# Performance work log

Measured on AMD Instinct MI355X. Metric: run time of the kernel, lower is better.

Reference implementation:

```python
import jax, jax.numpy as jnp
import numpy as np

N = 65536
NUM_STATE = 128
NUM_HIDDEN = 256
NUM_EMBED = 128


def setup_inputs() -> dict:
    key = jax.random.key(0)
    ks = jax.random.split(key, 8)
    s1 = jax.random.normal(ks[0], (N, NUM_STATE), dtype=jnp.float32)
    s2 = jax.random.normal(ks[1], (N, NUM_STATE), dtype=jnp.float32)
    # kaiming_normal_(fan_in, linear): std = 1/sqrt(fan_in)
    W1 = jax.random.normal(ks[2], (NUM_HIDDEN, NUM_STATE), dtype=jnp.float32) / np.sqrt(NUM_STATE)
    b1 = jnp.zeros((NUM_HIDDEN,), dtype=jnp.float32)
    W2 = jax.random.normal(ks[3], (NUM_HIDDEN, NUM_HIDDEN), dtype=jnp.float32) / np.sqrt(NUM_HIDDEN)
    b2 = jnp.zeros((NUM_HIDDEN,), dtype=jnp.float32)
    W3 = jax.random.normal(ks[4], (NUM_EMBED, NUM_HIDDEN), dtype=jnp.float32) / np.sqrt(NUM_HIDDEN)
    b3 = jnp.zeros((NUM_EMBED,), dtype=jnp.float32)
    return {"s1": s1, "s2": s2, "W1": W1, "b1": b1, "W2": W2, "b2": b2, "W3": W3, "b3": b3}


def _embed(x, W1, b1, W2, b2, W3, b3):
    h = jax.nn.selu(x @ W1.T + b1)
    h = jax.nn.selu(h @ W2.T + b2)
    return h @ W3.T + b3  # [N, num_embedding]


def reference(s1, s2, W1, b1, W2, b2, W3, b3):
    e1 = _embed(s1, W1, b1, W2, b2, W3, b3)
    e2 = _embed(s2, W1, b1, W2, b2, W3, b3)
    # diag(e1 @ e2.T) == per-row dot product (same math, O(N*d) not O(N^2*d))
    dots = jnp.einsum('nd,nd->n', e1, e2)
    out = dots / (jnp.linalg.norm(e1, axis=1) * jnp.linalg.norm(e2, axis=1))
    out = (out + 1.0) / 2.0
    return jax.nn.sigmoid(out)
```

## Files before the change

kernel.cpp:

```cpp
#include <hip/hip_runtime.h>


typedef __bf16 bf16x8 __attribute__((ext_vector_type(8)));
typedef __bf16 bf16x4 __attribute__((ext_vector_type(4)));
typedef float  f32x4  __attribute__((ext_vector_type(4)));

constexpr int WS_W1 = 0;
constexpr int WS_W2 = 32768;
constexpr int WS_W3 = 98304;

__device__ __forceinline__ float selu_f(float x) {
    const float scale = 1.0507009873554805f;
    const float sa    = 1.7580993408473766f;
    float xp = fmaxf(x, 0.f);
    float xn = fminf(x, 0.f);
    return fmaf(scale, xp, sa * (__expf(xn) - 1.f));
}

template<int COLS>
__device__ __forceinline__ bf16x8 read_act(const __bf16* lds, int row, int kcol) {
    unsigned byte = (unsigned)((row * COLS + kcol) * 2) ^ ((unsigned)(row & 7) << 4);
    return *(const bf16x8*)((const char*)lds + byte);
}

template<bool SELU, int COLS>
__device__ __forceinline__ void store_act(__bf16* lds, int row, int col0, f32x4 a) {
    float v0 = a[0], v1 = a[1], v2 = a[2], v3 = a[3];
    if (SELU) { v0 = selu_f(v0); v1 = selu_f(v1); v2 = selu_f(v2); v3 = selu_f(v3); }
    bf16x4 u;
    u[0] = (__bf16)v0; u[1] = (__bf16)v1; u[2] = (__bf16)v2; u[3] = (__bf16)v3;
    unsigned byte = (unsigned)((row * COLS + col0) * 2) ^ ((unsigned)(row & 7) << 4);
    *(bf16x4*)((char*)lds + byte) = u;
}

__global__ void pack_weights_kernel(const float* __restrict__ W1,
                                    const float* __restrict__ W2,
                                    const float* __restrict__ W3,
                                    __bf16* __restrict__ ws) {
    int t = blockIdx.x * blockDim.x + threadIdx.x;
    const float* W; int K, KS, f, base;
    if (t < 4096)       { W = W1; K = 128; KS = 4; f = t;         base = WS_W1; }
    else if (t < 12288) { W = W2; K = 256; KS = 8; f = t - 4096;  base = WS_W2; }
    else                { W = W3; K = 256; KS = 8; f = t - 12288; base = WS_W3; }
    int lane = f & 63;
    int ks   = (f >> 6) % KS;
    int ct   = f / (64 * KS);
    int row  = ct * 16 + (lane & 15);
    int k0   = ks * 32 + (lane >> 4) * 8;
    const float* src = W + (size_t)row * K + k0;
    __bf16* dst = ws + base + (size_t)f * 8;
#pragma unroll
    for (int j = 0; j < 8; ++j) dst[j] = (__bf16)src[j];
}

__global__ __launch_bounds__(256, 3)
void embed_sim_kernel(const float* __restrict__ s1, const float* __restrict__ s2,
                      const float* __restrict__ b1, const float* __restrict__ b2,
                      const float* __restrict__ b3,
                      const __bf16* __restrict__ wf, float* __restrict__ out) {
    __shared__ __align__(16) __bf16 Xs[64 * 128];
    __shared__ __align__(16) __bf16 hA[64 * 256];

    const int tid  = threadIdx.x;
    const int wave = tid >> 6;
    const int lane = tid & 63;
    const int lr   = lane & 15;
    const int kg   = lane >> 4;
    const int p0   = blockIdx.x * 32;

    __bf16* h2hi = hA;
    __bf16* Es   = hA + 64 * 128;

#pragma unroll
    for (int it = 0; it < 4; ++it) {
        int idx = tid + it * 256;
        int row = idx >> 4;
        int k0  = (idx & 15) << 3;
        const float* src = (row < 32) ? (s1 + (size_t)(p0 + row) * 128 + k0)
                                      : (s2 + (size_t)(p0 + row - 32) * 128 + k0);
        float4 v0 = *(const float4*)(src);
        float4 v1 = *(const float4*)(src + 4);
        bf16x8 w;
        w[0] = (__bf16)v0.x; w[1] = (__bf16)v0.y; w[2] = (__bf16)v0.z; w[3] = (__bf16)v0.w;
        w[4] = (__bf16)v1.x; w[5] = (__bf16)v1.y; w[6] = (__bf16)v1.z; w[7] = (__bf16)v1.w;
        unsigned byte = (unsigned)((row * 128 + k0) * 2) ^ ((unsigned)(row & 7) << 4);
        *(bf16x8*)((char*)Xs + byte) = w;
    }
    __syncthreads();

    {
        bf16x8 wfr[4][4]; f32x4 bv[4];
#pragma unroll
        for (int ti = 0; ti < 4; ++ti) {
            int t = wave * 4 + ti;
#pragma unroll
            for (int ks = 0; ks < 4; ++ks)
                wfr[ti][ks] = *(const bf16x8*)(wf + WS_W1 + (size_t)((t * 4 + ks) * 64 + lane) * 8);
            bv[ti] = *(const f32x4*)(b1 + t * 16 + kg * 4);
        }
#pragma unroll
        for (int s = 0; s < 4; ++s) {
            const int row = s * 16 + lr;
            bf16x8 xfr[4];
#pragma unroll
            for (int ks = 0; ks < 4; ++ks) xfr[ks] = read_act<128>(Xs, row, ks * 32 + kg * 8);
#pragma unroll
            for (int ti = 0; ti < 4; ++ti) {
                f32x4 acc = bv[ti];
#pragma unroll
                for (int ks = 0; ks < 4; ++ks)
                    acc = __builtin_amdgcn_mfma_f32_16x16x32_bf16(wfr[ti][ks], xfr[ks], acc, 0, 0, 0);
                store_act<true, 256>(hA, row, (wave * 4 + ti) * 16 + kg * 4, acc);
            }
        }
    }
    __syncthreads();

    {
        f32x4 acc[4][4];
#pragma unroll
        for (int ti = 0; ti < 4; ++ti) {
            f32x4 b = *(const f32x4*)(b2 + (wave * 4 + ti) * 16 + kg * 4);
#pragma unroll
            for (int s = 0; s < 4; ++s) acc[ti][s] = b;
        }
#pragma unroll
        for (int kh = 0; kh < 2; ++kh) {
            bf16x8 wfr[4][4];
#pragma unroll
            for (int ti = 0; ti < 4; ++ti) {
                int t = wave * 4 + ti;
#pragma unroll
                for (int ks = 0; ks < 4; ++ks)
                    wfr[ti][ks] = *(const bf16x8*)(wf + WS_W2 + (size_t)((t * 8 + kh * 4 + ks) * 64 + lane) * 8);
            }
#pragma unroll
            for (int s = 0; s < 4; ++s) {
                const int row = s * 16 + lr;
                bf16x8 hfr[4];
#pragma unroll
                for (int ks = 0; ks < 4; ++ks)
                    hfr[ks] = read_act<256>(hA, row, kh * 128 + ks * 32 + kg * 8);
#pragma unroll
                for (int ti = 0; ti < 4; ++ti)
#pragma unroll
                    for (int ks = 0; ks < 4; ++ks)
                        acc[ti][s] = __builtin_amdgcn_mfma_f32_16x16x32_bf16(
                            wfr[ti][ks], hfr[ks], acc[ti][s], 0, 0, 0);
            }
        }
        if (wave < 2) {
#pragma unroll
            for (int ti = 0; ti < 4; ++ti)
#pragma unroll
                for (int s = 0; s < 4; ++s)
                    store_act<true, 128>(Xs, s * 16 + lr, (wave * 4 + ti) * 16 + kg * 4, acc[ti][s]);
        }
        __syncthreads();
        if (wave >= 2) {
#pragma unroll
            for (int ti = 0; ti < 4; ++ti)
#pragma unroll
                for (int s = 0; s < 4; ++s)
                    store_act<true, 128>(h2hi, s * 16 + lr, ((wave - 2) * 4 + ti) * 16 + kg * 4, acc[ti][s]);
        }
    }
    __syncthreads();

    {
        f32x4 acc[2][4];
#pragma unroll
        for (int ti = 0; ti < 2; ++ti) {
            f32x4 b = *(const f32x4*)(b3 + (wave * 2 + ti) * 16 + kg * 4);
#pragma unroll
            for (int s = 0; s < 4; ++s) acc[ti][s] = b;
        }
#pragma unroll
        for (int kh = 0; kh < 2; ++kh) {
            const __bf16* src = (kh == 0) ? Xs : h2hi;
            bf16x8 wfr[2][4];
#pragma unroll
            for (int ti = 0; ti < 2; ++ti) {
                int t = wave * 2 + ti;
#pragma unroll
                for (int ks = 0; ks < 4; ++ks)
                    wfr[ti][ks] = *(const bf16x8*)(wf + WS_W3 + (size_t)((t * 8 + kh * 4 + ks) * 64 + lane) * 8);
            }
#pragma unroll
            for (int s = 0; s < 4; ++s) {
                const int row = s * 16 + lr;
                bf16x8 hfr[4];
#pragma unroll
                for (int ks = 0; ks < 4; ++ks)
                    hfr[ks] = read_act<128>(src, row, ks * 32 + kg * 8);
#pragma unroll
                for (int ti = 0; ti < 2; ++ti)
#pragma unroll
                    for (int ks = 0; ks < 4; ++ks)
                        acc[ti][s] = __builtin_amdgcn_mfma_f32_16x16x32_bf16(
                            wfr[ti][ks], hfr[ks], acc[ti][s], 0, 0, 0);
            }
        }
#pragma unroll
        for (int ti = 0; ti < 2; ++ti)
#pragma unroll
            for (int s = 0; s < 4; ++s)
                store_act<false, 128>(Es, s * 16 + lr, (wave * 2 + ti) * 16 + kg * 4, acc[ti][s]);
    }
    __syncthreads();

    const int p  = tid >> 3;
    const int dg = tid & 7;
    float dot = 0.f, n1 = 0.f, n2 = 0.f;
#pragma unroll
    for (int half = 0; half < 2; ++half) {
        int d0 = dg * 16 + half * 8;
        unsigned by1 = (unsigned)((p * 128 + d0) * 2) ^ ((unsigned)(p & 7) << 4);
        unsigned by2 = (unsigned)(((p + 32) * 128 + d0) * 2) ^ ((unsigned)((p + 32) & 7) << 4);
        bf16x8 e1 = *(const bf16x8*)((const char*)Es + by1);
        bf16x8 e2 = *(const bf16x8*)((const char*)Es + by2);
#pragma unroll
        for (int j = 0; j < 8; ++j) {
            float a = (float)e1[j], b = (float)e2[j];
            dot = fmaf(a, b, dot);
            n1  = fmaf(a, a, n1);
            n2  = fmaf(b, b, n2);
        }
    }
#pragma unroll
    for (int off = 1; off < 8; off <<= 1) {
        dot += __shfl_xor(dot, off);
        n1  += __shfl_xor(n1,  off);
        n2  += __shfl_xor(n2,  off);
    }
    if (dg == 0) {
        float r = dot * rsqrtf(n1 * n2);
        float x = (r + 1.f) * 0.5f;
        out[p0 + p] = 1.f / (1.f + __expf(-x));
    }
}

extern "C" void kernel_launch(void* const* d_in, const int* in_sizes, int n_in,
                              void* d_out, int out_size, void* d_ws, size_t ws_size,
                              hipStream_t stream) {
    const float* s1 = (const float*)d_in[0];
    const float* s2 = (const float*)d_in[1];
    const float* W1 = (const float*)d_in[2];
    const float* b1 = (const float*)d_in[3];
    const float* W2 = (const float*)d_in[4];
    const float* b2 = (const float*)d_in[5];
    const float* W3 = (const float*)d_in[6];
    const float* b3 = (const float*)d_in[7];
    __bf16* wf = (__bf16*)d_ws;
    float*  outp = (float*)d_out;

    pack_weights_kernel<<<64, 256, 0, stream>>>(W1, W2, W3, wf);

    const int npairs = in_sizes[0] / 128;
    embed_sim_kernel<<<npairs / 32, 256, 0, stream>>>(s1, s2, b1, b2, b3, wf, outp);
}
```

Measured before the change: 58.22 us.

## Compute cosine similarity from MFMA accumulators and add setprio around MFMA blocks

The final embedding is no longer written to LDS as bf16 and re-read for the per-row dot and norms. Partial dot and norm sums are taken straight from the layer-3 accumulators, reduced across lanes with shuffles, then summed over the four waves through a small fp32 LDS buffer. MFMA sections are wrapped in s_setprio to favour matrix issue, and SELU is rewritten with exp2f and an fma. The cosine is now computed in fp32 rather than on bf16-rounded embeddings, at the cost of an extra cross-wave reduction step.

```diff
diff --git a/kernel.cpp b/kernel.cpp
--- a/kernel.cpp
+++ b/kernel.cpp
@@ -12,9 +12,9 @@
 __device__ __forceinline__ float selu_f(float x) {
     const float scale = 1.0507009873554805f;
     const float sa    = 1.7580993408473766f;
-    float xp = fmaxf(x, 0.f);
-    float xn = fminf(x, 0.f);
-    return fmaf(scale, xp, sa * (__expf(xn) - 1.f));
+    const float l2e   = 1.4426950408889634f;
+    float e = exp2f(fminf(x, 0.f) * l2e);
+    return fmaf(scale, fmaxf(x, 0.f), fmaf(sa, e, -sa));
 }
 
 template<int COLS>
@@ -69,7 +69,7 @@
     const int p0   = blockIdx.x * 32;
 
     __bf16* h2hi = hA;
-    __bf16* Es   = hA + 64 * 128;
+    float*  red  = (float*)(hA + 64 * 128);
 
 #pragma unroll
     for (int it = 0; it < 4; ++it) {
@@ -107,9 +107,11 @@
 #pragma unroll
             for (int ti = 0; ti < 4; ++ti) {
                 f32x4 acc = bv[ti];
+                __builtin_amdgcn_s_setprio(1);
 #pragma unroll
                 for (int ks = 0; ks < 4; ++ks)
                     acc = __builtin_amdgcn_mfma_f32_16x16x32_bf16(wfr[ti][ks], xfr[ks], acc, 0, 0, 0);
+                __builtin_amdgcn_s_setprio(0);
                 store_act<true, 256>(hA, row, (wave * 4 + ti) * 16 + kg * 4, acc);
             }
         }
@@ -141,12 +143,14 @@
 #pragma unroll
                 for (int ks = 0; ks < 4; ++ks)
                     hfr[ks] = read_act<256>(hA, row, kh * 128 + ks * 32 + kg * 8);
+                __builtin_amdgcn_s_setprio(1);
 #pragma unroll
                 for (int ti = 0; ti < 4; ++ti)
 #pragma unroll
                     for (int ks = 0; ks < 4; ++ks)
                         acc[ti][s] = __builtin_amdgcn_mfma_f32_16x16x32_bf16(
                             wfr[ti][ks], hfr[ks], acc[ti][s], 0, 0, 0);
+                __builtin_amdgcn_s_setprio(0);
             }
         }
         if (wave < 2) {
@@ -167,13 +171,13 @@
     }
     __syncthreads();
 
-    {
-        f32x4 acc[2][4];
+    f32x4 acc3[2][4];
+    {
 #pragma unroll
         for (int ti = 0; ti < 2; ++ti) {
             f32x4 b = *(const f32x4*)(b3 + (wave * 2 + ti) * 16 + kg * 4);
 #pragma unroll
-            for (int s = 0; s < 4; ++s) acc[ti][s] = b;
+            for (int s = 0; s < 4; ++s) acc3[ti][s] = b;
         }
 #pragma unroll
         for (int kh = 0; kh < 2; ++kh) {
@@ -193,48 +197,53 @@
 #pragma unroll
                 for (int ks = 0; ks < 4; ++ks)
                     hfr[ks] = read_act<128>(src, row, ks * 32 + kg * 8);
+                __builtin_amdgcn_s_setprio(1);
 #pragma unroll
                 for (int ti = 0; ti < 2; ++ti)
 #pragma unroll
                     for (int ks = 0; ks < 4; ++ks)
-                        acc[ti][s] = __builtin_amdgcn_mfma_f32_16x16x32_bf16(
-                            wfr[ti][ks], hfr[ks], acc[ti][s], 0, 0, 0);
-            }
-        }
+                        acc3[ti][s] = __builtin_amdgcn_mfma_f32_16x16x32_bf16(
+                            wfr[ti][ks], hfr[ks], acc3[ti][s], 0, 0, 0);
+                __builtin_amdgcn_s_setprio(0);
+            }
+        }
+    }
+
+    {
+        float d0 = 0.f, a0 = 0.f, c0 = 0.f;
+        float d1 = 0.f, a1 = 0.f, c1 = 0.f;
 #pragma unroll
         for (int ti = 0; ti < 2; ++ti)
 #pragma unroll
-            for (int s = 0; s < 4; ++s)
-                store_act<false, 128>(Es, s * 16 + lr, (wave * 2 + ti) * 16 + kg * 4, acc[ti][s]);
-    }
-    __syncthreads();
-
-    const int p  = tid >> 3;
-    const int dg = tid & 7;
-    float dot = 0.f, n1 = 0.f, n2 = 0.f;
-#pragma unroll
-    for (int half = 0; half < 2; ++half) {
-        int d0 = dg * 16 + half * 8;
-        unsigned by1 = (unsigned)((p * 128 + d0) * 2) ^ ((unsigned)(p & 7) << 4);
-        unsigned by2 = (unsigned)(((p + 32) * 128 + d0) * 2) ^ ((unsigned)((p + 32) & 7) << 4);
-        bf16x8 e1 = *(const bf16x8*)((const char*)Es + by1);
-        bf16x8 e2 = *(const bf16x8*)((const char*)Es + by2);
-#pragma unroll
-        for (int j = 0; j < 8; ++j) {
-            float a = (float)e1[j], b = (float)e2[j];
-            dot = fmaf(a, b, dot);
-            n1  = fmaf(a, a, n1);
-            n2  = fmaf(b, b, n2);
-        }
-    }
-#pragma unroll
-    for (int off = 1; off < 8; off <<= 1) {
-        dot += __shfl_xor(dot, off);
-        n1  += __shfl_xor(n1,  off);
-        n2  += __shfl_xor(n2,  off);
-    }
-    if (dg == 0) {
-        float r = dot * rsqrtf(n1 * n2);
+            for (int j = 0; j < 4; ++j) {
+                float e1a = acc3[ti][0][j], e2a = acc3[ti][2][j];
+                float e1b = acc3[ti][1][j], e2b = acc3[ti][3][j];
+                d0 = fmaf(e1a, e2a, d0); a0 = fmaf(e1a, e1a, a0); c0 = fmaf(e2a, e2a, c0);
+                d1 = fmaf(e1b, e2b, d1); a1 = fmaf(e1b, e1b, a1); c1 = fmaf(e2b, e2b, c1);
+            }
+#pragma unroll
+        for (int off = 16; off < 64; off <<= 1) {
+            d0 += __shfl_xor(d0, off); a0 += __shfl_xor(a0, off); c0 += __shfl_xor(c0, off);
+            d1 += __shfl_xor(d1, off); a1 += __shfl_xor(a1, off); c1 += __shfl_xor(c1, off);
+        }
+        if (kg == 0) {
+            float* r0 = red + ((wave * 32) + lr) * 3;
+            r0[0] = d0; r0[1] = a0; r0[2] = c0;
+            float* r1 = red + ((wave * 32) + 16 + lr) * 3;
+            r1[0] = d1; r1[1] = a1; r1[2] = c1;
+        }
+    }
+    __syncthreads();
+
+    if (tid < 32) {
+        const int p = tid;
+        float D = 0.f, A = 0.f, C = 0.f;
+#pragma unroll
+        for (int w = 0; w < 4; ++w) {
+            const float* r = red + ((w * 32) + p) * 3;
+            D += r[0]; A += r[1]; C += r[2];
+        }
+        float r = D * rsqrtf(A * C);
         float x = (r + 1.f) * 0.5f;
         out[p0 + p] = 1.f / (1.f + __expf(-x));
     }
```

Result: slower. 63.17 us (+8.5%).
